# Performance work log

Hardware: AMD Instinct MI355X
Metric: run time of the kernel (lower is better)

Reference implementation:

```python
import jax, jax.numpy as jnp
import numpy as np

H, E, K = 1024, 8, 2  # hidden_size, num_experts, top_k
B, S = 2, 4096


def setup_inputs() -> dict:
    key = jax.random.key(0)
    ks = jax.random.split(key, 5)
    s = 1.0 / np.sqrt(H)
    return {
        "x": jax.random.normal(ks[0], (B, S, H), dtype=jnp.float32),
        "ln_scale": jnp.ones((H,), jnp.float32),
        "ln_bias": jnp.zeros((H,), jnp.float32),
        "w1": (jax.random.normal(ks[1], (H, H), jnp.float32) * s),
        "b1": jnp.zeros((H,), jnp.float32),
        "w2": (jax.random.normal(ks[2], (H, E), jnp.float32) * s),
        "b2": jnp.zeros((E,), jnp.float32),
        "We": (jax.random.normal(ks[3], (E, H, H), jnp.float32) * s),
        "be": jnp.zeros((E, H), jnp.float32),
    }


def _layernorm(x, scale, bias, eps=1e-5):
    m = jnp.mean(x, axis=-1, keepdims=True)
    v = jnp.var(x, axis=-1, keepdims=True)
    return (x - m) * jax.lax.rsqrt(v + eps) * scale + bias


def reference(x, ln_scale, ln_bias, w1, b1, w2, b2, We, be):
    b, s, h = x.shape
    # --- router (BaseRouter): LN -> MLP -> softmax -> top-k -> renorm ---
    xn = _layernorm(x, ln_scale, ln_bias)
    hmid = jax.nn.relu(xn @ w1 + b1)
    logits = hmid @ w2 + b2                      # [B,S,E]
    probs = jax.nn.softmax(logits, axis=-1)
    topk_p, topk_i = jax.lax.top_k(probs, K)     # [B,S,K]
    topk_p = topk_p / jnp.sum(topk_p, axis=-1, keepdims=True)
    # sparse combine weights [B,S,E]: renormalized top-k gate, 0 elsewhere
    cw = jnp.sum(topk_p[..., None] * jax.nn.one_hot(topk_i, E, dtype=x.dtype), axis=-2)
    # --- expert dispatch / weighted combine ---
    t = b * s
    xf = x.reshape(t, h)
    cwf = cw.reshape(t, E)
    ye = jnp.einsum('th,ehd->etd', xf, We) + be[:, None, :]   # [E,T,H]
    out = jnp.einsum('te,etd->td', cwf, ye).reshape(b, s, h)
    # --- aux load-balance loss ---
    mean_p = jnp.mean(probs, axis=(0, 1))        # [E]
    aux = jnp.sum(mean_p * jnp.log(mean_p * E + 1e-9))
    return out, aux
```

## Files before the change

### kernel.cpp

```cpp
#include <hip/hip_runtime.h>
#include <hip/hip_fp16.h>

#define H 1024
#define E 8
#define TT 8192

typedef __attribute__((ext_vector_type(8))) short bf16x8;
typedef __attribute__((ext_vector_type(4))) float f32x4;

__device__ __forceinline__ unsigned short f2bf(float f) {
  unsigned int u = __float_as_uint(f);
  u += 0x7fffu + ((u >> 16) & 1u);
  return (unsigned short)(u >> 16);
}

__device__ __forceinline__ int swz(int row, int c) {
  return (row << 5) | (((c ^ (row >> 1)) & 3) << 3);
}

__device__ __forceinline__ void gld16(void* lds, const void* g) {
  __builtin_amdgcn_global_load_lds((const __attribute__((address_space(1))) void*)g,
                                   (__attribute__((address_space(3))) void*)lds, 16, 0, 0);
}

__global__ __launch_bounds__(64) void k_init(int* cnt, double* psum) {
  int t = threadIdx.x;
  if (t < E) { cnt[t] = 0; psum[t] = 0.0; }
}

__global__ __launch_bounds__(256) void k_cast_we(const float* __restrict__ we, unsigned short* __restrict__ wet) {
  __shared__ unsigned short tile[32][33];
  int e = blockIdx.z;
  int kb = blockIdx.x << 5, nb = blockIdx.y << 5;
  int t = threadIdx.x;
  int cc = t & 31, rr = t >> 5;
  size_t base = (size_t)e * H * H;
#pragma unroll
  for (int r = 0; r < 4; ++r) {
    int k = kb + rr + (r << 3);
    tile[rr + (r << 3)][cc] = f2bf(we[base + (size_t)k * H + nb + cc]);
  }
  __syncthreads();
#pragma unroll
  for (int r = 0; r < 4; ++r) {
    int n = nb + rr + (r << 3);
    wet[base + (size_t)n * H + kb + cc] = tile[cc][rr + (r << 3)];
  }
}

__global__ __launch_bounds__(256) void k_cast_w1(const float* __restrict__ w1, const float* __restrict__ lsc,
                                                 unsigned short* __restrict__ w1h, unsigned short* __restrict__ w1l) {
  __shared__ float tile[32][33];
  int kb = blockIdx.x << 5, nb = blockIdx.y << 5;
  int t = threadIdx.x;
  int cc = t & 31, rr = t >> 5;
#pragma unroll
  for (int r = 0; r < 4; ++r) {
    int k = kb + rr + (r << 3);
    tile[rr + (r << 3)][cc] = w1[(size_t)k * H + nb + cc] * lsc[k];
  }
  __syncthreads();
#pragma unroll
  for (int r = 0; r < 4; ++r) {
    int n = nb + rr + (r << 3);
    float v = tile[cc][rr + (r << 3)];
    unsigned short h = f2bf(v);
    float hv = __uint_as_float((unsigned)h << 16);
    unsigned short l = f2bf(v - hv);
    w1h[(size_t)n * H + kb + cc] = h;
    w1l[(size_t)n * H + kb + cc] = l;
  }
}

__global__ __launch_bounds__(256) void k_b1a(const float* __restrict__ w1, const float* __restrict__ lbi,
                                             float* __restrict__ part) {
  int bk = blockIdx.x, t = threadIdx.x;
  float a0 = 0, a1 = 0, a2 = 0, a3 = 0;
  for (int kk = 0; kk < 16; ++kk) {
    int k = (bk << 4) + kk;
    float lb = lbi[k];
    const float* row = &w1[(size_t)k * H];
    a0 = fmaf(lb, row[t], a0);
    a1 = fmaf(lb, row[t + 256], a1);
    a2 = fmaf(lb, row[t + 512], a2);
    a3 = fmaf(lb, row[t + 768], a3);
  }
  part[bk * H + t] = a0;
  part[bk * H + t + 256] = a1;
  part[bk * H + t + 512] = a2;
  part[bk * H + t + 768] = a3;
}

__global__ __launch_bounds__(256) void k_b1b(const float* __restrict__ part, const float* __restrict__ b1,
                                             float* __restrict__ b1eff) {
  int n = (blockIdx.x << 8) + threadIdx.x;
  float s = b1[n];
  for (int j = 0; j < 64; ++j) s += part[j * H + n];
  b1eff[n] = s;
}

__global__ __launch_bounds__(256) void k_stats(const float* __restrict__ x, unsigned short* __restrict__ xb,
                                               unsigned short* __restrict__ zh, unsigned short* __restrict__ zl) {
  int tok = blockIdx.x, t = threadIdx.x;
  const float4 v = *reinterpret_cast<const float4*>(&x[(size_t)tok * H + (t << 2)]);
  float s = v.x + v.y + v.z + v.w;
  float ss = v.x * v.x + v.y * v.y + v.z * v.z + v.w * v.w;
#pragma unroll
  for (int off = 32; off; off >>= 1) { s += __shfl_down(s, off); ss += __shfl_down(ss, off); }
  __shared__ float red[4][2];
  int lane = t & 63, wv = t >> 6;
  if (lane == 0) { red[wv][0] = s; red[wv][1] = ss; }
  __syncthreads();
  float fs = red[0][0] + red[1][0] + red[2][0] + red[3][0];
  float fss = red[0][1] + red[1][1] + red[2][1] + red[3][1];
  float mean = fs * (1.0f / H);
  float var = fss * (1.0f / H) - mean * mean;
  float rstd = rsqrtf(var + 1e-5f);
  float mb = -mean * rstd;
  size_t base = (size_t)tok * H + (t << 2);
  ushort4 ob;
  ob.x = f2bf(v.x); ob.y = f2bf(v.y); ob.z = f2bf(v.z); ob.w = f2bf(v.w);
  *reinterpret_cast<ushort4*>(&xb[base]) = ob;
  float zz[4];
  zz[0] = fmaf(v.x, rstd, mb); zz[1] = fmaf(v.y, rstd, mb);
  zz[2] = fmaf(v.z, rstd, mb); zz[3] = fmaf(v.w, rstd, mb);
  ushort4 oh, ol;
  unsigned u0 = __float_as_uint(zz[0]), u1 = __float_as_uint(zz[1]);
  unsigned u2 = __float_as_uint(zz[2]), u3 = __float_as_uint(zz[3]);
  oh.x = (unsigned short)(u0 >> 16); oh.y = (unsigned short)(u1 >> 16);
  oh.z = (unsigned short)(u2 >> 16); oh.w = (unsigned short)(u3 >> 16);
  float l0 = zz[0] - __uint_as_float(u0 & 0xffff0000u);
  float l1 = zz[1] - __uint_as_float(u1 & 0xffff0000u);
  float l2 = zz[2] - __uint_as_float(u2 & 0xffff0000u);
  float l3 = zz[3] - __uint_as_float(u3 & 0xffff0000u);
  ol.x = (unsigned short)(__float_as_uint(l0) >> 16); ol.y = (unsigned short)(__float_as_uint(l1) >> 16);
  ol.z = (unsigned short)(__float_as_uint(l2) >> 16); ol.w = (unsigned short)(__float_as_uint(l3) >> 16);
  *reinterpret_cast<ushort4*>(&zh[base]) = oh;
  *reinterpret_cast<ushort4*>(&zl[base]) = ol;
}

__global__ __launch_bounds__(256) void k_router_mfma(
    const unsigned short* __restrict__ zh, const unsigned short* __restrict__ zl,
    const unsigned short* __restrict__ w1h,
    const float* __restrict__ b1eff, const float* __restrict__ w2, float* __restrict__ plog) {
  __shared__ __align__(16) short Bt[3][8192];
  int t = threadIdx.x;
  int d = blockIdx.x;
  int l = ((d & 7) << 6) + (d >> 3);
  int bm = (l >> 3) << 7;
  int bnb = l & 7, bn = bnb << 7;
  int w = t >> 6, lane = t & 63;
  int l15 = lane & 15, lgp = lane >> 4;
  int wr = (w >> 1) << 6, wc = (w & 1) << 6;
  int sl = (w << 8) + lane;
  int bo[4];
#pragma unroll
  for (int q = 0; q < 4; ++q) {
    int s = sl + (q << 6);
    int r = s >> 2, cg = (s & 3) ^ ((r >> 1) & 3);
    bo[q] = ((r < 128) ? (bn + r) * H : 1048576 + (bn + r - 128) * H) + (cg << 3);
  }
  int dB = w << 11;
  int zo[4];
#pragma unroll
  for (int i = 0; i < 4; ++i) zo[i] = (bm + wr + (i << 4) + l15) * H + (lgp << 3);
  f32x4 acc[4][4];
#pragma unroll
  for (int i = 0; i < 4; ++i)
#pragma unroll
    for (int j = 0; j < 4; ++j) acc[i][j] = f32x4{0.f, 0.f, 0.f, 0.f};
  bf16x8 ah[3][4], al[3][4];
#pragma unroll
  for (int q = 0; q < 4; ++q) gld16(&Bt[0][dB + (q << 9)], w1h + bo[q]);
#pragma unroll
  for (int q = 0; q < 4; ++q) gld16(&Bt[1][dB + (q << 9)], w1h + bo[q] + 32);
#pragma unroll
  for (int i = 0; i < 4; ++i) {
    ah[0][i] = *(const bf16x8*)(zh + zo[i]);
    al[0][i] = *(const bf16x8*)(zl + zo[i]);
    ah[1][i] = *(const bf16x8*)(zh + zo[i] + 32);
    al[1][i] = *(const bf16x8*)(zl + zo[i] + 32);
  }
#pragma unroll
  for (int kt = 0; kt < 32; ++kt) {
    const int cur = kt % 3;
    if (kt <= 29) {
      const int slot = (kt + 2) % 3, ko = (kt + 2) << 5;
#pragma unroll
      for (int i = 0; i < 4; ++i) {
        ah[slot][i] = *(const bf16x8*)(zh + zo[i] + ko);
        al[slot][i] = *(const bf16x8*)(zl + zo[i] + ko);
      }
    }
    if (kt <= 29) {
      asm volatile("s_waitcnt vmcnt(20)" ::: "memory");
    } else if (kt == 30) {
      asm volatile("s_waitcnt vmcnt(12)" ::: "memory");
    } else {
      asm volatile("s_waitcnt vmcnt(0)" ::: "memory");
    }
    __builtin_amdgcn_sched_barrier(0);
    __builtin_amdgcn_s_barrier();
    __builtin_amdgcn_sched_barrier(0);
    if (kt <= 29) {
      const int bnxt = (kt + 2) % 3, ko = (kt + 2) << 5;
#pragma unroll
      for (int q = 0; q < 4; ++q) gld16(&Bt[bnxt][dB + (q << 9)], w1h + bo[q] + ko);
    }
#pragma unroll
    for (int j = 0; j < 4; ++j) {
      bf16x8 bh = *(const bf16x8*)&Bt[cur][swz(wc + (j << 4) + l15, lgp)];
      bf16x8 bl = *(const bf16x8*)&Bt[cur][swz(128 + wc + (j << 4) + l15, lgp)];
#pragma unroll
      for (int i = 0; i < 4; ++i) {
        acc[i][j] = __builtin_amdgcn_mfma_f32_16x16x32_bf16(ah[cur][i], bh, acc[i][j], 0, 0, 0);
        acc[i][j] = __builtin_amdgcn_mfma_f32_16x16x32_bf16(ah[cur][i], bl, acc[i][j], 0, 0, 0);
        acc[i][j] = __builtin_amdgcn_mfma_f32_16x16x32_bf16(al[cur][i], bh, acc[i][j], 0, 0, 0);
      }
    }
  }
  float w2r[4][8], b1r[4];
#pragma unroll
  for (int j = 0; j < 4; ++j) {
    int col = bn + wc + (j << 4) + l15;
    float4 p0 = *(const float4*)&w2[(size_t)col * E];
    float4 p1 = *(const float4*)&w2[(size_t)col * E + 4];
    w2r[j][0] = p0.x; w2r[j][1] = p0.y; w2r[j][2] = p0.z; w2r[j][3] = p0.w;
    w2r[j][4] = p1.x; w2r[j][5] = p1.y; w2r[j][6] = p1.z; w2r[j][7] = p1.w;
    b1r[j] = b1eff[col];
  }
#pragma unroll
  for (int i = 0; i < 4; ++i)
#pragma unroll
    for (int j = 0; j < 4; ++j)
#pragma unroll
      for (int r = 0; r < 4; ++r) acc[i][j][r] = fmaxf(acc[i][j][r] + b1r[j], 0.f);
  int wh = wc >> 6;
  size_t pbase = ((size_t)(bnb * 2 + wh) * TT + bm) * E;
#pragma unroll
  for (int e = 0; e < E; ++e) {
    float se[4][4];
#pragma unroll
    for (int i = 0; i < 4; ++i)
#pragma unroll
      for (int r = 0; r < 4; ++r)
        se[i][r] = acc[i][0][r] * w2r[0][e] + acc[i][1][r] * w2r[1][e] +
                   acc[i][2][r] * w2r[2][e] + acc[i][3][r] * w2r[3][e];
#pragma unroll
    for (int off = 1; off < 16; off <<= 1)
#pragma unroll
      for (int i = 0; i < 4; ++i)
#pragma unroll
        for (int r = 0; r < 4; ++r) se[i][r] += __shfl_xor(se[i][r], off);
    if (l15 == 0) {
#pragma unroll
      for (int i = 0; i < 4; ++i)
#pragma unroll
        for (int r = 0; r < 4; ++r) {
          int row = wr + (i << 4) + (lgp << 2) + r;
          plog[pbase + (size_t)row * E + e] = se[i][r];
        }
    }
  }
}

__global__ __launch_bounds__(256) void k_top(const float* __restrict__ plog, const float* __restrict__ b2,
                                             int* __restrict__ topE, float* __restrict__ topW,
                                             int* __restrict__ listIdx, float* __restrict__ listW,
                                             int* __restrict__ cnt, double* __restrict__ psum) {
  int t = threadIdx.x, lane = t & 63;
  int tok = (blockIdx.x << 8) + t;
  float lg[E], p[E];
  float4 ba = *reinterpret_cast<const float4*>(b2);
  float4 bb = *reinterpret_cast<const float4*>(b2 + 4);
  lg[0] = ba.x; lg[1] = ba.y; lg[2] = ba.z; lg[3] = ba.w;
  lg[4] = bb.x; lg[5] = bb.y; lg[6] = bb.z; lg[7] = bb.w;
#pragma unroll
  for (int nb = 0; nb < 16; ++nb) {
    const float* pp = &plog[((size_t)nb * TT + tok) * E];
    float4 q0 = *reinterpret_cast<const float4*>(pp);
    float4 q1 = *reinterpret_cast<const float4*>(pp + 4);
    lg[0] += q0.x; lg[1] += q0.y; lg[2] += q0.z; lg[3] += q0.w;
    lg[4] += q1.x; lg[5] += q1.y; lg[6] += q1.z; lg[7] += q1.w;
  }
  float m = lg[0];
#pragma unroll
  for (int e = 1; e < E; ++e) m = fmaxf(m, lg[e]);
  float s = 0.f;
#pragma unroll
  for (int e = 0; e < E; ++e) { p[e] = __expf(lg[e] - m); s += p[e]; }
  float inv = 1.f / s;
#pragma unroll
  for (int e = 0; e < E; ++e) p[e] *= inv;
  {
    float ps[E];
#pragma unroll
    for (int e = 0; e < E; ++e) ps[e] = p[e];
#pragma unroll
    for (int off = 1; off < 64; off <<= 1)
#pragma unroll
      for (int e = 0; e < E; ++e) ps[e] += __shfl_xor(ps[e], off);
    if (lane == 0)
#pragma unroll
      for (int e = 0; e < E; ++e) atomicAdd(&psum[e], (double)ps[e]);
  }
  int e0 = 0;
#pragma unroll
  for (int e = 1; e < E; ++e) if (p[e] > p[e0]) e0 = e;
  int e1 = (e0 == 0) ? 1 : 0;
#pragma unroll
  for (int e = 0; e < E; ++e) if (e != e0 && p[e] > p[e1]) e1 = e;
  float rsw = 1.f / (p[e0] + p[e1]);
  float w0 = p[e0] * rsw, w1v = p[e1] * rsw;
  topE[tok << 1] = e0; topE[(tok << 1) + 1] = e1;
  topW[tok << 1] = w0; topW[(tok << 1) + 1] = w1v;
  unsigned long long lt = (1ull << lane) - 1ull;
#pragma unroll
  for (int e = 0; e < E; ++e) {
    unsigned long long m0 = __ballot(e0 == e);
    unsigned long long m1 = __ballot(e1 == e);
    int n0 = __popcll(m0), total = n0 + __popcll(m1);
    if (total == 0) continue;
    int leader = __ffsll(m0 | m1) - 1;
    int base = 0;
    if (lane == leader) base = atomicAdd(&cnt[e], total);
    base = __shfl(base, leader);
    if (e0 == e) {
      int pos = e * TT + base + __popcll(m0 & lt);
      listIdx[pos] = (tok << 1); listW[pos] = w0;
    }
    if (e1 == e) {
      int pos = e * TT + base + n0 + __popcll(m1 & lt);
      listIdx[pos] = (tok << 1) | 1; listW[pos] = w1v;
    }
  }
}

#define WL_SLOTS 2560
__global__ __launch_bounds__(256) void k_sched(const int* __restrict__ cnt, int* __restrict__ workList) {
  int t = threadIdx.x;
  for (int i = t; i < WL_SLOTS; i += 256) workList[i] = -1;
  __syncthreads();
  if (t < E) {
    int e = t;
    int nb = (cnt[e] + 127) >> 7;
    int ov = 2048 + (e << 6);
    int g = 0;
    for (int bx = 0; bx < nb; ++bx) {
      for (int by = 0; by < 8; ++by) {
        int item = (e << 12) | (bx << 4) | by;
        int slot = (g < 256) ? ((g << 3) + e) : ov++;
        workList[slot] = item;
        ++g;
      }
    }
  }
}

__global__ __launch_bounds__(256) void k_expert_gemm(const unsigned short* __restrict__ xb,
                                                     const unsigned short* __restrict__ wet,
                                                     const int* __restrict__ listIdx, const float* __restrict__ listW,
                                                     const int* __restrict__ cnt, const int* __restrict__ workList,
                                                     unsigned short* __restrict__ ys) {
  int item = workList[blockIdx.x];
  if (item < 0) return;
  int e = item >> 12, bx = (item >> 4) & 255, by = item & 15;
  int c = cnt[e];
  int r0 = bx << 7, n0 = by << 7;
  __shared__ __align__(16) short A[2][4096], Bs[2][4096];
  __shared__ int gi[128];
  __shared__ float gw[128];
  int t = threadIdx.x;
  if (t < 128) {
    int rr = r0 + t;
    gi[t] = (rr < c) ? listIdx[e * TT + rr] : -1;
    gw[t] = (rr < c) ? listW[e * TT + rr] : 0.f;
  }
  __syncthreads();
  int w = t >> 6, lane = t & 63;
  int l15 = lane & 15, lgp = lane >> 4;
  int wr = (w >> 1) << 6, wc = (w & 1) << 6;
  int s0 = (w << 7) + lane, s1 = s0 + 64;
  int rA0 = s0 >> 2, cg0 = (s0 & 3) ^ ((rA0 >> 1) & 3);
  int rA1 = s1 >> 2, cg1 = (s1 & 3) ^ ((rA1 >> 1) & 3);
  int pk0 = gi[rA0], pk1 = gi[rA1];
  const unsigned short* srcA0 = xb + (size_t)((pk0 < 0) ? 0 : (pk0 >> 1)) * H + (cg0 << 3);
  const unsigned short* srcA1 = xb + (size_t)((pk1 < 0) ? 0 : (pk1 >> 1)) * H + (cg1 << 3);
  size_t wbase = (size_t)e * H * H;
  const unsigned short* srcB0 = wet + wbase + (size_t)(n0 + rA0) * H + (cg0 << 3);
  const unsigned short* srcB1 = wet + wbase + (size_t)(n0 + rA1) * H + (cg1 << 3);
  int d0 = (w << 10), d1 = d0 + 512;
  f32x4 acc[4][4];
#pragma unroll
  for (int i = 0; i < 4; ++i)
#pragma unroll
    for (int j = 0; j < 4; ++j) acc[i][j] = f32x4{0.f, 0.f, 0.f, 0.f};
  gld16(&A[0][d0], srcA0); gld16(&A[0][d1], srcA1);
  gld16(&Bs[0][d0], srcB0); gld16(&Bs[0][d1], srcB1);
#pragma unroll
  for (int kt = 0; kt < 32; ++kt) {
    const int cur = kt & 1, nxt = cur ^ 1;
    if (kt < 31) {
      const int ko = (kt + 1) << 5;
      gld16(&A[nxt][d0], srcA0 + ko); gld16(&A[nxt][d1], srcA1 + ko);
      gld16(&Bs[nxt][d0], srcB0 + ko); gld16(&Bs[nxt][d1], srcB1 + ko);
      asm volatile("s_waitcnt vmcnt(4)" ::: "memory");
    } else {
      asm volatile("s_waitcnt vmcnt(0)" ::: "memory");
    }
    __builtin_amdgcn_sched_barrier(0);
    __builtin_amdgcn_s_barrier();
    __builtin_amdgcn_sched_barrier(0);
    bf16x8 bq[4];
#pragma unroll
    for (int j = 0; j < 4; ++j) bq[j] = *(const bf16x8*)&Bs[cur][swz(wc + (j << 4) + l15, lgp)];
    bf16x8 aq[4];
#pragma unroll
    for (int i = 0; i < 4; ++i) aq[i] = *(const bf16x8*)&A[cur][swz(wr + (i << 4) + l15, lgp)];
    __builtin_amdgcn_s_setprio(1);
#pragma unroll
    for (int i = 0; i < 4; ++i)
#pragma unroll
      for (int j = 0; j < 4; ++j)
        acc[i][j] = __builtin_amdgcn_mfma_f32_16x16x32_bf16(aq[i], bq[j], acc[i][j], 0, 0, 0);
    __builtin_amdgcn_s_setprio(0);
    if (kt < 31) {
      __builtin_amdgcn_sched_barrier(0);
      __builtin_amdgcn_s_barrier();
    }
  }
#pragma unroll
  for (int i = 0; i < 4; ++i) {
#pragma unroll
    for (int r = 0; r < 4; ++r) {
      int row = wr + (i << 4) + (lgp << 2) + r;
      int pk = gi[row];
      if (pk < 0) continue;
      int tok = pk >> 1, slot = pk & 1;
      float wgt = gw[row];
      size_t ob = ((size_t)slot * TT + tok) * H + n0 + wc + l15;
#pragma unroll
      for (int j = 0; j < 4; ++j) ys[ob + (j << 4)] = __half_as_ushort(__float2half(wgt * acc[i][j][r]));
    }
  }
}

__global__ __launch_bounds__(256) void k_combine(const unsigned short* __restrict__ ys, const int* __restrict__ topE,
                                                 const float* __restrict__ topW, const float* __restrict__ be,
                                                 float* __restrict__ out) {
  int tok = blockIdx.x, t = threadIdx.x;
  int e0 = topE[tok << 1], e1 = topE[(tok << 1) + 1];
  float w0 = topW[tok << 1], w1v = topW[(tok << 1) + 1];
  int h = t << 2;
  size_t base = (size_t)tok * H + h;
  ushort4 a = *reinterpret_cast<const ushort4*>(&ys[base]);
  ushort4 b = *reinterpret_cast<const ushort4*>(&ys[(size_t)TT * H + base]);
  float4 b0 = *reinterpret_cast<const float4*>(&be[e0 * H + h]);
  float4 b1v = *reinterpret_cast<const float4*>(&be[e1 * H + h]);
  float4 o;
  o.x = __half2float(__ushort_as_half(a.x)) + __half2float(__ushort_as_half(b.x)) + w0 * b0.x + w1v * b1v.x;
  o.y = __half2float(__ushort_as_half(a.y)) + __half2float(__ushort_as_half(b.y)) + w0 * b0.y + w1v * b1v.y;
  o.z = __half2float(__ushort_as_half(a.z)) + __half2float(__ushort_as_half(b.z)) + w0 * b0.z + w1v * b1v.z;
  o.w = __half2float(__ushort_as_half(a.w)) + __half2float(__ushort_as_half(b.w)) + w0 * b0.w + w1v * b1v.w;
  *reinterpret_cast<float4*>(&out[base]) = o;
}

__global__ __launch_bounds__(64) void k_aux(const double* __restrict__ psum, float* __restrict__ outAux) {
  if (threadIdx.x == 0) {
    double a = 0.0;
    for (int e = 0; e < E; ++e) {
      double mp = psum[e] / (double)TT;
      a += mp * log(mp * (double)E + 1e-9);
    }
    outAux[0] = (float)a;
  }
}

extern "C" void kernel_launch(void* const* d_in, const int* in_sizes, int n_in, void* d_out, int out_size, void* d_ws,
                              size_t ws_size, hipStream_t stream) {
  const float* x = (const float*)d_in[0];
  const float* lsc = (const float*)d_in[1];
  const float* lbi = (const float*)d_in[2];
  const float* w1 = (const float*)d_in[3];
  const float* b1 = (const float*)d_in[4];
  const float* w2 = (const float*)d_in[5];
  const float* b2 = (const float*)d_in[6];
  const float* we = (const float*)d_in[7];
  const float* be = (const float*)d_in[8];
  float* out = (float*)d_out;
  char* ws = (char*)d_ws;

  char* p = ws;
  int* topE = (int*)p; p += TT * 2 * 4;
  float* topW = (float*)p; p += TT * 2 * 4;
  int* listIdx = (int*)p; p += E * TT * 4;
  float* listW = (float*)p; p += E * TT * 4;
  int* cnt = (int*)p; p += 256;
  double* psum = (double*)p; p += 2048;
  float* b1eff = (float*)p; p += H * 4;
  float* part = (float*)p; p += 64 * H * 4;
  int* workList = (int*)p; p += WL_SLOTS * 4;
  unsigned short* xb = (unsigned short*)(ws + (2ull << 20));
  unsigned short* zh = (unsigned short*)(ws + (18ull << 20));
  unsigned short* zl = (unsigned short*)(ws + (34ull << 20));
  unsigned short* w1h = (unsigned short*)(ws + (50ull << 20));
  unsigned short* w1l = (unsigned short*)(ws + (52ull << 20));
  float* plog = (float*)(ws + (54ull << 20));
  unsigned short* wet = (unsigned short*)(ws + (18ull << 20));
  unsigned short* ys = (unsigned short*)(ws + (34ull << 20));

  k_init<<<1, 64, 0, stream>>>(cnt, psum);
  k_cast_w1<<<dim3(32, 32), 256, 0, stream>>>(w1, lsc, w1h, w1l);
  k_b1a<<<64, 256, 0, stream>>>(w1, lbi, part);
  k_b1b<<<4, 256, 0, stream>>>(part, b1, b1eff);
  k_stats<<<TT, 256, 0, stream>>>(x, xb, zh, zl);
  k_router_mfma<<<512, 256, 0, stream>>>(zh, zl, w1h, b1eff, w2, plog);
  k_top<<<TT / 256, 256, 0, stream>>>(plog, b2, topE, topW, listIdx, listW, cnt, psum);
  k_sched<<<1, 256, 0, stream>>>(cnt, workList);
  k_cast_we<<<dim3(32, 32, E), 256, 0, stream>>>(we, wet);
  k_expert_gemm<<<WL_SLOTS, 256, 0, stream>>>(xb, wet, listIdx, listW, cnt, workList, ys);
  k_combine<<<TT, 256, 0, stream>>>(ys, topE, topW, be, out);
  k_aux<<<1, 64, 0, stream>>>(psum, out + (size_t)TT * H);
}
```

Measured before the change: 245.3 us.

## Fuse bias-fold into w1 cast, shrink router tiles, register-prefetch expert GEMM A operand

The k_init and k_b1a kernels are folded into k_cast_w1 and k_b1b, removing launches and a separate read of w1. The router GEMM moves to 128x64 tiles with twice as many blocks and addresses w1l through its own pointer. The expert GEMM now loads gathered activation rows straight into registers with a 4-deep prefetch, triple-buffers B in LDS and drops the second barrier per iteration. Together these aim to cut launch overhead and memory stalls, at the cost of more partial logits (32 slices) in k_top and a larger work list.

```diff
diff --git a/kernel.cpp b/kernel.cpp
--- a/kernel.cpp
+++ b/kernel.cpp
@@ -21,11 +21,6 @@
 __device__ __forceinline__ void gld16(void* lds, const void* g) {
   __builtin_amdgcn_global_load_lds((const __attribute__((address_space(1))) void*)g,
                                    (__attribute__((address_space(3))) void*)lds, 16, 0, 0);
-}
-
-__global__ __launch_bounds__(64) void k_init(int* cnt, double* psum) {
-  int t = threadIdx.x;
-  if (t < E) { cnt[t] = 0; psum[t] = 0.0; }
 }
 
 __global__ __launch_bounds__(256) void k_cast_we(const float* __restrict__ we, unsigned short* __restrict__ wet) {
@@ -49,21 +44,38 @@
 }
 
 __global__ __launch_bounds__(256) void k_cast_w1(const float* __restrict__ w1, const float* __restrict__ lsc,
-                                                 unsigned short* __restrict__ w1h, unsigned short* __restrict__ w1l) {
+                                                 const float* __restrict__ lbi, unsigned short* __restrict__ w1h,
+                                                 unsigned short* __restrict__ w1l, float* __restrict__ part) {
   __shared__ float tile[32][33];
+  __shared__ float red[8][33];
   int kb = blockIdx.x << 5, nb = blockIdx.y << 5;
   int t = threadIdx.x;
   int cc = t & 31, rr = t >> 5;
 #pragma unroll
   for (int r = 0; r < 4; ++r) {
     int k = kb + rr + (r << 3);
-    tile[rr + (r << 3)][cc] = w1[(size_t)k * H + nb + cc] * lsc[k];
+    tile[rr + (r << 3)][cc] = w1[(size_t)k * H + nb + cc];
   }
   __syncthreads();
+  float pp = 0.f;
+#pragma unroll
+  for (int r = 0; r < 4; ++r) {
+    int kk = rr + (r << 3);
+    pp = fmaf(lbi[kb + kk], tile[kk][cc], pp);
+  }
+  red[rr][cc] = pp;
+  float scale = lsc[kb + cc];
+  __syncthreads();
+  if (rr == 0) {
+    float s = 0.f;
+#pragma unroll
+    for (int j = 0; j < 8; ++j) s += red[j][cc];
+    part[blockIdx.x * H + nb + cc] = s;
+  }
 #pragma unroll
   for (int r = 0; r < 4; ++r) {
     int n = nb + rr + (r << 3);
-    float v = tile[cc][rr + (r << 3)];
+    float v = tile[cc][rr + (r << 3)] * scale;
     unsigned short h = f2bf(v);
     float hv = __uint_as_float((unsigned)h << 16);
     unsigned short l = f2bf(v - hv);
@@ -72,31 +84,15 @@
   }
 }
 
-__global__ __launch_bounds__(256) void k_b1a(const float* __restrict__ w1, const float* __restrict__ lbi,
-                                             float* __restrict__ part) {
-  int bk = blockIdx.x, t = threadIdx.x;
-  float a0 = 0, a1 = 0, a2 = 0, a3 = 0;
-  for (int kk = 0; kk < 16; ++kk) {
-    int k = (bk << 4) + kk;
-    float lb = lbi[k];
-    const float* row = &w1[(size_t)k * H];
-    a0 = fmaf(lb, row[t], a0);
-    a1 = fmaf(lb, row[t + 256], a1);
-    a2 = fmaf(lb, row[t + 512], a2);
-    a3 = fmaf(lb, row[t + 768], a3);
-  }
-  part[bk * H + t] = a0;
-  part[bk * H + t + 256] = a1;
-  part[bk * H + t + 512] = a2;
-  part[bk * H + t + 768] = a3;
-}
-
 __global__ __launch_bounds__(256) void k_b1b(const float* __restrict__ part, const float* __restrict__ b1,
-                                             float* __restrict__ b1eff) {
-  int n = (blockIdx.x << 8) + threadIdx.x;
+                                             float* __restrict__ b1eff, int* __restrict__ cnt,
+                                             double* __restrict__ psum) {
+  int t = threadIdx.x;
+  int n = (blockIdx.x << 8) + t;
   float s = b1[n];
-  for (int j = 0; j < 64; ++j) s += part[j * H + n];
+  for (int j = 0; j < 32; ++j) s += part[j * H + n];
   b1eff[n] = s;
+  if (blockIdx.x == 0 && t < E) { cnt[t] = 0; psum[t] = 0.0; }
 }
 
 __global__ __launch_bounds__(256) void k_stats(const float* __restrict__ x, unsigned short* __restrict__ xb,
@@ -141,43 +137,40 @@
 
 __global__ __launch_bounds__(256) void k_router_mfma(
     const unsigned short* __restrict__ zh, const unsigned short* __restrict__ zl,
-    const unsigned short* __restrict__ w1h,
+    const unsigned short* __restrict__ w1h, const unsigned short* __restrict__ w1l,
     const float* __restrict__ b1eff, const float* __restrict__ w2, float* __restrict__ plog) {
-  __shared__ __align__(16) short Bt[3][8192];
+  __shared__ __align__(16) short Bt[3][4096];
   int t = threadIdx.x;
   int d = blockIdx.x;
-  int l = ((d & 7) << 6) + (d >> 3);
-  int bm = (l >> 3) << 7;
-  int bnb = l & 7, bn = bnb << 7;
+  int l = ((d & 7) << 7) + (d >> 3);
+  int bm = (l >> 4) << 7;
+  int bnb = l & 15, bn = bnb << 6;
   int w = t >> 6, lane = t & 63;
   int l15 = lane & 15, lgp = lane >> 4;
-  int wr = (w >> 1) << 6, wc = (w & 1) << 6;
-  int sl = (w << 8) + lane;
-  int bo[4];
-#pragma unroll
-  for (int q = 0; q < 4; ++q) {
-    int s = sl + (q << 6);
+  int wr = (w >> 1) << 6, wc = (w & 1) << 5;
+  const unsigned short* srcB[2];
+#pragma unroll
+  for (int q = 0; q < 2; ++q) {
+    int s = t + (q << 8);
     int r = s >> 2, cg = (s & 3) ^ ((r >> 1) & 3);
-    bo[q] = ((r < 128) ? (bn + r) * H : 1048576 + (bn + r - 128) * H) + (cg << 3);
-  }
-  int dB = w << 11;
+    srcB[q] = ((r < 64) ? &w1h[(size_t)(bn + r) * H] : &w1l[(size_t)(bn + r - 64) * H]) + (cg << 3);
+  }
+  int dB0 = t << 3, dB1 = dB0 + 2048;
   int zo[4];
 #pragma unroll
   for (int i = 0; i < 4; ++i) zo[i] = (bm + wr + (i << 4) + l15) * H + (lgp << 3);
-  f32x4 acc[4][4];
+  f32x4 acc[4][2];
 #pragma unroll
   for (int i = 0; i < 4; ++i)
 #pragma unroll
-    for (int j = 0; j < 4; ++j) acc[i][j] = f32x4{0.f, 0.f, 0.f, 0.f};
+    for (int j = 0; j < 2; ++j) acc[i][j] = f32x4{0.f, 0.f, 0.f, 0.f};
   bf16x8 ah[3][4], al[3][4];
-#pragma unroll
-  for (int q = 0; q < 4; ++q) gld16(&Bt[0][dB + (q << 9)], w1h + bo[q]);
-#pragma unroll
-  for (int q = 0; q < 4; ++q) gld16(&Bt[1][dB + (q << 9)], w1h + bo[q] + 32);
+  gld16(&Bt[0][dB0], srcB[0]); gld16(&Bt[0][dB1], srcB[1]);
+#pragma unroll
+  for (int i = 0; i < 4; ++i) { ah[0][i] = *(const bf16x8*)(zh + zo[i]); al[0][i] = *(const bf16x8*)(zl + zo[i]); }
+  gld16(&Bt[1][dB0], srcB[0] + 32); gld16(&Bt[1][dB1], srcB[1] + 32);
 #pragma unroll
   for (int i = 0; i < 4; ++i) {
-    ah[0][i] = *(const bf16x8*)(zh + zo[i]);
-    al[0][i] = *(const bf16x8*)(zl + zo[i]);
     ah[1][i] = *(const bf16x8*)(zh + zo[i] + 32);
     al[1][i] = *(const bf16x8*)(zl + zo[i] + 32);
   }
@@ -193,9 +186,9 @@
       }
     }
     if (kt <= 29) {
-      asm volatile("s_waitcnt vmcnt(20)" ::: "memory");
+      asm volatile("s_waitcnt vmcnt(18)" ::: "memory");
     } else if (kt == 30) {
-      asm volatile("s_waitcnt vmcnt(12)" ::: "memory");
+      asm volatile("s_waitcnt vmcnt(10)" ::: "memory");
     } else {
       asm volatile("s_waitcnt vmcnt(0)" ::: "memory");
     }
@@ -204,24 +197,28 @@
     __builtin_amdgcn_sched_barrier(0);
     if (kt <= 29) {
       const int bnxt = (kt + 2) % 3, ko = (kt + 2) << 5;
-#pragma unroll
-      for (int q = 0; q < 4; ++q) gld16(&Bt[bnxt][dB + (q << 9)], w1h + bo[q] + ko);
-    }
-#pragma unroll
-    for (int j = 0; j < 4; ++j) {
-      bf16x8 bh = *(const bf16x8*)&Bt[cur][swz(wc + (j << 4) + l15, lgp)];
-      bf16x8 bl = *(const bf16x8*)&Bt[cur][swz(128 + wc + (j << 4) + l15, lgp)];
-#pragma unroll
-      for (int i = 0; i < 4; ++i) {
-        acc[i][j] = __builtin_amdgcn_mfma_f32_16x16x32_bf16(ah[cur][i], bh, acc[i][j], 0, 0, 0);
-        acc[i][j] = __builtin_amdgcn_mfma_f32_16x16x32_bf16(ah[cur][i], bl, acc[i][j], 0, 0, 0);
-        acc[i][j] = __builtin_amdgcn_mfma_f32_16x16x32_bf16(al[cur][i], bh, acc[i][j], 0, 0, 0);
+      gld16(&Bt[bnxt][dB0], srcB[0] + ko); gld16(&Bt[bnxt][dB1], srcB[1] + ko);
+    }
+    bf16x8 bh[2], bl[2];
+#pragma unroll
+    for (int j = 0; j < 2; ++j) {
+      bh[j] = *(const bf16x8*)&Bt[cur][swz(wc + (j << 4) + l15, lgp)];
+      bl[j] = *(const bf16x8*)&Bt[cur][swz(64 + wc + (j << 4) + l15, lgp)];
+    }
+    __builtin_amdgcn_s_setprio(1);
+#pragma unroll
+    for (int i = 0; i < 4; ++i)
+#pragma unroll
+      for (int j = 0; j < 2; ++j) {
+        acc[i][j] = __builtin_amdgcn_mfma_f32_16x16x32_bf16(ah[cur][i], bh[j], acc[i][j], 0, 0, 0);
+        acc[i][j] = __builtin_amdgcn_mfma_f32_16x16x32_bf16(ah[cur][i], bl[j], acc[i][j], 0, 0, 0);
+        acc[i][j] = __builtin_amdgcn_mfma_f32_16x16x32_bf16(al[cur][i], bh[j], acc[i][j], 0, 0, 0);
       }
-    }
-  }
-  float w2r[4][8], b1r[4];
-#pragma unroll
-  for (int j = 0; j < 4; ++j) {
+    __builtin_amdgcn_s_setprio(0);
+  }
+  float w2r[2][8], b1r[2];
+#pragma unroll
+  for (int j = 0; j < 2; ++j) {
     int col = bn + wc + (j << 4) + l15;
     float4 p0 = *(const float4*)&w2[(size_t)col * E];
     float4 p1 = *(const float4*)&w2[(size_t)col * E + 4];
@@ -232,10 +229,10 @@
 #pragma unroll
   for (int i = 0; i < 4; ++i)
 #pragma unroll
-    for (int j = 0; j < 4; ++j)
+    for (int j = 0; j < 2; ++j)
 #pragma unroll
       for (int r = 0; r < 4; ++r) acc[i][j][r] = fmaxf(acc[i][j][r] + b1r[j], 0.f);
-  int wh = wc >> 6;
+  int wh = wc >> 5;
   size_t pbase = ((size_t)(bnb * 2 + wh) * TT + bm) * E;
 #pragma unroll
   for (int e = 0; e < E; ++e) {
@@ -244,8 +241,7 @@
     for (int i = 0; i < 4; ++i)
 #pragma unroll
       for (int r = 0; r < 4; ++r)
-        se[i][r] = acc[i][0][r] * w2r[0][e] + acc[i][1][r] * w2r[1][e] +
-                   acc[i][2][r] * w2r[2][e] + acc[i][3][r] * w2r[3][e];
+        se[i][r] = acc[i][0][r] * w2r[0][e] + acc[i][1][r] * w2r[1][e];
 #pragma unroll
     for (int off = 1; off < 16; off <<= 1)
 #pragma unroll
@@ -276,7 +272,7 @@
   lg[0] = ba.x; lg[1] = ba.y; lg[2] = ba.z; lg[3] = ba.w;
   lg[4] = bb.x; lg[5] = bb.y; lg[6] = bb.z; lg[7] = bb.w;
 #pragma unroll
-  for (int nb = 0; nb < 16; ++nb) {
+  for (int nb = 0; nb < 32; ++nb) {
     const float* pp = &plog[((size_t)nb * TT + tok) * E];
     float4 q0 = *reinterpret_cast<const float4*>(pp);
     float4 q1 = *reinterpret_cast<const float4*>(pp + 4);
@@ -336,7 +332,7 @@
   }
 }
 
-#define WL_SLOTS 2560
+#define WL_SLOTS 4096
 __global__ __launch_bounds__(256) void k_sched(const int* __restrict__ cnt, int* __restrict__ workList) {
   int t = threadIdx.x;
   for (int i = t; i < WL_SLOTS; i += 256) workList[i] = -1;
@@ -344,12 +340,11 @@
   if (t < E) {
     int e = t;
     int nb = (cnt[e] + 127) >> 7;
-    int ov = 2048 + (e << 6);
     int g = 0;
     for (int bx = 0; bx < nb; ++bx) {
       for (int by = 0; by < 8; ++by) {
         int item = (e << 12) | (bx << 4) | by;
-        int slot = (g < 256) ? ((g << 3) + e) : ov++;
+        int slot = (g < 256) ? ((g << 3) + e) : (2048 + (e << 8) + (g - 256));
         workList[slot] = item;
         ++g;
       }
@@ -367,7 +362,7 @@
   int e = item >> 12, bx = (item >> 4) & 255, by = item & 15;
   int c = cnt[e];
   int r0 = bx << 7, n0 = by << 7;
-  __shared__ __align__(16) short A[2][4096], Bs[2][4096];
+  __shared__ __align__(16) short Bs[3][4096];
   __shared__ int gi[128];
   __shared__ float gw[128];
   int t = threadIdx.x;
@@ -380,54 +375,69 @@
   int w = t >> 6, lane = t & 63;
   int l15 = lane & 15, lgp = lane >> 4;
   int wr = (w >> 1) << 6, wc = (w & 1) << 6;
-  int s0 = (w << 7) + lane, s1 = s0 + 64;
-  int rA0 = s0 >> 2, cg0 = (s0 & 3) ^ ((rA0 >> 1) & 3);
-  int rA1 = s1 >> 2, cg1 = (s1 & 3) ^ ((rA1 >> 1) & 3);
-  int pk0 = gi[rA0], pk1 = gi[rA1];
-  const unsigned short* srcA0 = xb + (size_t)((pk0 < 0) ? 0 : (pk0 >> 1)) * H + (cg0 << 3);
-  const unsigned short* srcA1 = xb + (size_t)((pk1 < 0) ? 0 : (pk1 >> 1)) * H + (cg1 << 3);
   size_t wbase = (size_t)e * H * H;
-  const unsigned short* srcB0 = wet + wbase + (size_t)(n0 + rA0) * H + (cg0 << 3);
-  const unsigned short* srcB1 = wet + wbase + (size_t)(n0 + rA1) * H + (cg1 << 3);
-  int d0 = (w << 10), d1 = d0 + 512;
+  const unsigned short* srcB[2];
+#pragma unroll
+  for (int q = 0; q < 2; ++q) {
+    int s = t + (q << 8);
+    int r = s >> 2, cg = (s & 3) ^ ((r >> 1) & 3);
+    srcB[q] = wet + wbase + (size_t)(n0 + r) * H + (cg << 3);
+  }
+  int dB0 = t << 3, dB1 = dB0 + 2048;
+  int ao[4];
+#pragma unroll
+  for (int i = 0; i < 4; ++i) {
+    int pk = gi[wr + (i << 4) + l15];
+    ao[i] = ((pk < 0) ? 0 : (pk >> 1)) * H + (lgp << 3);
+  }
   f32x4 acc[4][4];
 #pragma unroll
   for (int i = 0; i < 4; ++i)
 #pragma unroll
     for (int j = 0; j < 4; ++j) acc[i][j] = f32x4{0.f, 0.f, 0.f, 0.f};
-  gld16(&A[0][d0], srcA0); gld16(&A[0][d1], srcA1);
-  gld16(&Bs[0][d0], srcB0); gld16(&Bs[0][d1], srcB1);
+  bf16x8 a[4][4];
+  gld16(&Bs[0][dB0], srcB[0]); gld16(&Bs[0][dB1], srcB[1]);
+#pragma unroll
+  for (int i = 0; i < 4; ++i) a[0][i] = *(const bf16x8*)(xb + ao[i]);
+  gld16(&Bs[1][dB0], srcB[0] + 32); gld16(&Bs[1][dB1], srcB[1] + 32);
+#pragma unroll
+  for (int i = 0; i < 4; ++i) a[1][i] = *(const bf16x8*)(xb + ao[i] + 32);
+#pragma unroll
+  for (int i = 0; i < 4; ++i) a[2][i] = *(const bf16x8*)(xb + ao[i] + 64);
 #pragma unroll
   for (int kt = 0; kt < 32; ++kt) {
-    const int cur = kt & 1, nxt = cur ^ 1;
-    if (kt < 31) {
-      const int ko = (kt + 1) << 5;
-      gld16(&A[nxt][d0], srcA0 + ko); gld16(&A[nxt][d1], srcA1 + ko);
-      gld16(&Bs[nxt][d0], srcB0 + ko); gld16(&Bs[nxt][d1], srcB1 + ko);
-      asm volatile("s_waitcnt vmcnt(4)" ::: "memory");
+    const int curA = kt & 3, curB = kt % 3;
+    if (kt <= 28) {
+      const int slot = (kt + 3) & 3, ko = (kt + 3) << 5;
+#pragma unroll
+      for (int i = 0; i < 4; ++i) a[slot][i] = *(const bf16x8*)(xb + ao[i] + ko);
+    }
+    if (kt <= 28) {
+      asm volatile("s_waitcnt vmcnt(10)" ::: "memory");
+    } else if (kt == 29) {
+      asm volatile("s_waitcnt vmcnt(6)" ::: "memory");
+    } else if (kt == 30) {
+      asm volatile("s_waitcnt vmcnt(2)" ::: "memory");
     } else {
       asm volatile("s_waitcnt vmcnt(0)" ::: "memory");
     }
     __builtin_amdgcn_sched_barrier(0);
     __builtin_amdgcn_s_barrier();
     __builtin_amdgcn_sched_barrier(0);
+    if (kt <= 29) {
+      const int bnxt = (kt + 2) % 3, ko = (kt + 2) << 5;
+      gld16(&Bs[bnxt][dB0], srcB[0] + ko); gld16(&Bs[bnxt][dB1], srcB[1] + ko);
+    }
     bf16x8 bq[4];
 #pragma unroll
-    for (int j = 0; j < 4; ++j) bq[j] = *(const bf16x8*)&Bs[cur][swz(wc + (j << 4) + l15, lgp)];
-    bf16x8 aq[4];
-#pragma unroll
-    for (int i = 0; i < 4; ++i) aq[i] = *(const bf16x8*)&A[cur][swz(wr + (i << 4) + l15, lgp)];
+    for (int j = 0; j < 4; ++j) bq[j] = *(const bf16x8*)&Bs[curB][swz(wc + (j << 4) + l15, lgp)];
     __builtin_amdgcn_s_setprio(1);
 #pragma unroll
     for (int i = 0; i < 4; ++i)
 #pragma unroll
       for (int j = 0; j < 4; ++j)
-        acc[i][j] = __builtin_amdgcn_mfma_f32_16x16x32_bf16(aq[i], bq[j], acc[i][j], 0, 0, 0);
+        acc[i][j] = __builtin_amdgcn_mfma_f32_16x16x32_bf16(a[curA][i], bq[j], acc[i][j], 0, 0, 0);
     __builtin_amdgcn_s_setprio(0);
-    if (kt < 31) {
-      __builtin_amdgcn_sched_barrier(0);
-      __builtin_amdgcn_s_barrier();
-    }
   }
 #pragma unroll
   for (int i = 0; i < 4; ++i) {
@@ -498,7 +508,7 @@
   int* cnt = (int*)p; p += 256;
   double* psum = (double*)p; p += 2048;
   float* b1eff = (float*)p; p += H * 4;
-  float* part = (float*)p; p += 64 * H * 4;
+  float* part = (float*)p; p += 32 * H * 4;
   int* workList = (int*)p; p += WL_SLOTS * 4;
   unsigned short* xb = (unsigned short*)(ws + (2ull << 20));
   unsigned short* zh = (unsigned short*)(ws + (18ull << 20));
@@ -509,12 +519,10 @@
   unsigned short* wet = (unsigned short*)(ws + (18ull << 20));
   unsigned short* ys = (unsigned short*)(ws + (34ull << 20));
 
-  k_init<<<1, 64, 0, stream>>>(cnt, psum);
-  k_cast_w1<<<dim3(32, 32), 256, 0, stream>>>(w1, lsc, w1h, w1l);
-  k_b1a<<<64, 256, 0, stream>>>(w1, lbi, part);
-  k_b1b<<<4, 256, 0, stream>>>(part, b1, b1eff);
+  k_cast_w1<<<dim3(32, 32), 256, 0, stream>>>(w1, lsc, lbi, w1h, w1l, part);
+  k_b1b<<<4, 256, 0, stream>>>(part, b1, b1eff, cnt, psum);
   k_stats<<<TT, 256, 0, stream>>>(x, xb, zh, zl);
-  k_router_mfma<<<512, 256, 0, stream>>>(zh, zl, w1h, b1eff, w2, plog);
+  k_router_mfma<<<1024, 256, 0, stream>>>(zh, zl, w1h, w1l, b1eff, w2, plog);
   k_top<<<TT / 256, 256, 0, stream>>>(plog, b2, topE, topW, listIdx, listW, cnt, psum);
   k_sched<<<1, 256, 0, stream>>>(cnt, workList);
   k_cast_we<<<dim3(32, 32, E), 256, 0, stream>>>(we, wet);
```

New measurement: 386.1 us. 1.57x slower.
